# Kernel optimization log

Hardware: AMD Instinct MI355X
Metric: run time of the kernel (lower is better)

## Reference

```python
import jax, jax.numpy as jnp
import numpy as np

B, GNN_DIM, TR_DIM, F = 16384, 512, 768, 1024


def setup_inputs() -> dict:
    key = jax.random.key(0)
    ks = jax.random.split(key, 16)
    s = 0.02
    return {
        "gnn_features": jax.random.normal(ks[0], (B, GNN_DIM), jnp.float32),
        "transformer_features": jax.random.normal(ks[1], (B, TR_DIM), jnp.float32),
        # gnn_projector / transformer_projector (torch Linear: y = x @ W.T + b)
        "Wg": jax.random.normal(ks[2], (F, GNN_DIM), jnp.float32) * s,
        "bg": jnp.zeros((F,), jnp.float32),
        "Wt": jax.random.normal(ks[3], (F, TR_DIM), jnp.float32) * s,
        "bt": jnp.zeros((F,), jnp.float32),
        # MultiheadAttention value-projection slice of in_proj_weight and out_proj.
        # With seq_len==1 the softmax over a single key is identically 1, so the
        # attention output is exactly out_proj(v_proj(key)); Q/K projections do
        # not affect the output (their gradients are exactly zero).
        "Wv": jax.random.normal(ks[4], (F, F), jnp.float32) * s,
        "bv": jnp.zeros((F,), jnp.float32),
        "Wo": jax.random.normal(ks[5], (F, F), jnp.float32) * s,
        "bo": jnp.zeros((F,), jnp.float32),
        # fusion_layers: Linear(2F -> F), GELU, Dropout(eval: identity), Linear(F -> F)
        "W1": jax.random.normal(ks[6], (F, 2 * F), jnp.float32) * s,
        "b1": jnp.zeros((F,), jnp.float32),
        "W2": jax.random.normal(ks[7], (F, F), jnp.float32) * s,
        "b2": jnp.zeros((F,), jnp.float32),
    }


def reference(gnn_features, transformer_features, Wg, bg, Wt, bt, Wv, bv, Wo, bo, W1, b1, W2, b2):
    # projections to fusion space  [B, F]
    gnn_proj = gnn_features @ Wg.T + bg
    tr_proj = transformer_features @ Wt.T + bt
    # degenerate single-token cross-attention: softmax over 1 key == 1, so
    # attn(q, k, v=k) = out_proj(v_proj(k)) regardless of the query.
    gnn_attended = (tr_proj @ Wv.T + bv) @ Wo.T + bo   # attention(gnn_seq, tr_seq, tr_seq)
    tr_attended = (gnn_proj @ Wv.T + bv) @ Wo.T + bo   # attention(tr_seq, gnn_seq, gnn_seq)
    combined = jnp.concatenate([gnn_attended, tr_attended], axis=-1)  # [B, 2F]
    h = jax.nn.gelu(combined @ W1.T + b1, approximate=False)          # exact GELU (torch default)
    fused = h @ W2.T + b2
    return fused + gnn_proj + tr_proj
```

## Files before the change

kernel.cpp:

```cpp
#include <hip/hip_runtime.h>
#include <cmath>

#define GAS __attribute__((address_space(1)))
#define LAS __attribute__((address_space(3)))

typedef __bf16 bf16x8 __attribute__((ext_vector_type(8)));
typedef float f32x4 __attribute__((ext_vector_type(4)));

__device__ __forceinline__ void gload16(const void* g, void* l) {
    __builtin_amdgcn_global_load_lds((const GAS void*)g, (LAS void*)l, 16, 0, 0);
}

__global__ void k_prep_convert(const float* __restrict__ gnn, const float* __restrict__ tr,
                               const float* __restrict__ Wo, const float* __restrict__ W1,
                               const float* __restrict__ W2, const float* __restrict__ Wg,
                               const float* __restrict__ Wt,
                               __bf16* __restrict__ X, __bf16* __restrict__ Wo_b,
                               __bf16* __restrict__ W1ab, __bf16* __restrict__ Wp) {
    int b = blockIdx.x;
    const float* src; __bf16* dst; int sld, dld, base, c8;
    if (b < 4096)       { src = gnn;       sld = 512;  dst = X + 1024;        dld = 2304; base = 0;     c8 = 64; }
    else if (b < 10240) { src = tr;        sld = 768;  dst = X + 1536;        dld = 2304; base = 4096;  c8 = 96; }
    else if (b < 10752) { src = Wo;        sld = 1024; dst = Wo_b;            dld = 1024; base = 10240; c8 = 128; }
    else if (b < 11264) { src = W1;        sld = 2048; dst = W1ab;            dld = 1024; base = 10752; c8 = 128; }
    else if (b < 11776) { src = W1 + 1024; sld = 2048; dst = W1ab + 1024*1024; dld = 1024; base = 11264; c8 = 128; }
    else if (b < 12288) { src = W2;        sld = 1024; dst = Wp;              dld = 2304; base = 11776; c8 = 128; }
    else if (b < 12544) { src = Wg;        sld = 512;  dst = Wp + 1024;       dld = 2304; base = 12288; c8 = 64; }
    else                { src = Wt;        sld = 768;  dst = Wp + 1536;       dld = 2304; base = 12544; c8 = 96; }
    int idx = (b - base) * 256 + threadIdx.x;
    int r = idx / c8;
    int c = (idx - r * c8) << 3;
    const float4* s = reinterpret_cast<const float4*>(src + (long)r * sld + c);
    float4 x0 = s[0], x1 = s[1];
    bf16x8 v;
    v[0] = (__bf16)x0.x; v[1] = (__bf16)x0.y; v[2] = (__bf16)x0.z; v[3] = (__bf16)x0.w;
    v[4] = (__bf16)x1.x; v[5] = (__bf16)x1.y; v[6] = (__bf16)x1.z; v[7] = (__bf16)x1.w;
    *reinterpret_cast<bf16x8*>(dst + (long)r * dld + c) = v;
}

__global__ void k_prep_transpose(const float* __restrict__ Wv, const float* __restrict__ Wg,
                                 const float* __restrict__ Wt,
                                 __bf16* __restrict__ WvT, __bf16* __restrict__ WgT,
                                 __bf16* __restrict__ WtT) {
    __shared__ float t[32][33];
    int b = blockIdx.x;
    const float* src; __bf16* dst; int R, C, tile;
    if (b < 1024)      { src = Wv; dst = WvT; R = 1024; C = 1024; tile = b; }
    else if (b < 1536) { src = Wg; dst = WgT; R = 1024; C = 512;  tile = b - 1024; }
    else               { src = Wt; dst = WtT; R = 1024; C = 768;  tile = b - 1536; }
    int tx_n = C >> 5;
    int c0 = (tile % tx_n) << 5, r0 = (tile / tx_n) << 5;
    int tx = threadIdx.x, ty = threadIdx.y;
    #pragma unroll
    for (int i = 0; i < 32; i += 8)
        t[ty + i][tx] = src[(long)(r0 + ty + i) * C + c0 + tx];
    __syncthreads();
    #pragma unroll
    for (int i = 0; i < 32; i += 8)
        dst[(long)(c0 + ty + i) * R + r0 + tx] = (__bf16)t[tx][ty + i];
}

__global__ void k_bias_att(const float* __restrict__ Wo, const float* __restrict__ bv,
                           const float* __restrict__ bo, float* __restrict__ b_att) {
    int i = blockIdx.x;
    float s = 0.f;
    for (int k = threadIdx.x; k < 1024; k += 256) s += Wo[i * 1024 + k] * bv[k];
    __shared__ float red[256];
    red[threadIdx.x] = s;
    __syncthreads();
    for (int off = 128; off > 0; off >>= 1) {
        if (threadIdx.x < off) red[threadIdx.x] += red[threadIdx.x + off];
        __syncthreads();
    }
    if (threadIdx.x == 0) b_att[i] = red[0] + bo[i];
}

__global__ void k_bias_z2(const float* __restrict__ W1, const float* __restrict__ b_att,
                          const float* __restrict__ b1,
                          const __bf16* __restrict__ P, const __bf16* __restrict__ Q,
                          const float* __restrict__ bt, const float* __restrict__ bg,
                          const float* __restrict__ b2,
                          float* __restrict__ bz2, float* __restrict__ b_out) {
    int i = blockIdx.x;
    float s = 0.f;
    for (int k = threadIdx.x; k < 1024; k += 256) {
        s += (W1[(long)i * 2048 + k] + W1[(long)i * 2048 + 1024 + k]) * b_att[k];
        s += (float)P[i * 1024 + k] * bt[k];
        s += (float)Q[i * 1024 + k] * bg[k];
    }
    __shared__ float red[256];
    red[threadIdx.x] = s;
    __syncthreads();
    for (int off = 128; off > 0; off >>= 1) {
        if (threadIdx.x < off) red[threadIdx.x] += red[threadIdx.x + off];
        __syncthreads();
    }
    if (threadIdx.x == 0) {
        bz2[i] = red[0] + b1[i];
        b_out[i] = b2[i] + bg[i] + bt[i];
    }
}

template <int BM, int BN>
__global__ __launch_bounds__(256, 2) void k_gemm_nt(
    const __bf16* __restrict__ A, int lda,
    const __bf16* __restrict__ B, int ldb,
    __bf16* __restrict__ C, int ldc,
    int K, int n_tiles) {
    constexpr int BK = 32;
    constexpr int MR = BM / 32, NR = BN / 32;
    __shared__ alignas(16) __bf16 As[2][BM][BK];
    __shared__ alignas(16) __bf16 Bs[2][BN][BK];

    const int tid = threadIdx.x;
    const int lane = tid & 63;
    const int wave = tid >> 6;
    int bid = blockIdx.x;
    const int nwg = gridDim.x;
    if ((nwg & 7) == 0) bid = (bid & 7) * (nwg >> 3) + (bid >> 3);
    const int bn = bid % n_tiles;
    const int bm = bid / n_tiles;
    const int m0 = bm * BM, n0 = bn * BN;

    const int rp_l = tid >> 2;
    const int sp = tid & 3;

    const int wr = (wave >> 1) * (BM / 2);
    const int wc = (wave & 1) * (BN / 2);
    const int fr = lane & 15;
    const int fb = (lane >> 4) << 4;

    f32x4 acc[MR][NR] = {};
    const int nk = K / BK;

    auto stage = [&](int buf, int kt) {
        char* abase = (char*)&As[buf][0][0];
        char* bbase = (char*)&Bs[buf][0][0];
        #pragma unroll
        for (int it = 0; it < BM / 64; ++it) {
            int rp = it * 64 + rp_l;
            int rl = (rp & ~1) | ((rp ^ (rp >> 2)) & 1);
            int sl = sp ^ (rl & 3);
            gload16(A + (long)(m0 + rl) * lda + kt * BK + sl * 8,
                    abase + it * 4096 + tid * 16);
        }
        #pragma unroll
        for (int it = 0; it < BN / 64; ++it) {
            int rp = it * 64 + rp_l;
            int rl = (rp & ~1) | ((rp ^ (rp >> 2)) & 1);
            int sl = sp ^ (rl & 3);
            gload16(B + (long)(n0 + rl) * ldb + kt * BK + sl * 8,
                    bbase + it * 4096 + tid * 16);
        }
    };

    stage(0, 0);
    for (int kt = 0; kt < nk; ++kt) {
        const int buf = kt & 1;
        __syncthreads();
        if (kt + 1 < nk) stage(buf ^ 1, kt + 1);
        const char* abase = (const char*)&As[buf][0][0];
        const char* bbase = (const char*)&Bs[buf][0][0];
        bf16x8 af[MR], bfr[NR];
        #pragma unroll
        for (int m = 0; m < MR; ++m) {
            int r = wr + m * 16 + fr;
            af[m] = *(const bf16x8*)(abase + (((r << 6) + fb) ^ ((r & 7) << 4)));
        }
        #pragma unroll
        for (int n = 0; n < NR; ++n) {
            int r = wc + n * 16 + fr;
            bfr[n] = *(const bf16x8*)(bbase + (((r << 6) + fb) ^ ((r & 7) << 4)));
        }
        #pragma unroll
        for (int m = 0; m < MR; ++m)
            #pragma unroll
            for (int n = 0; n < NR; ++n)
                acc[m][n] = __builtin_amdgcn_mfma_f32_16x16x32_bf16(af[m], bfr[n], acc[m][n], 0, 0, 0);
    }

    const int r0 = (lane >> 4) << 2;
    #pragma unroll
    for (int n = 0; n < NR; ++n) {
        const int gc = n0 + wc + n * 16 + fr;
        #pragma unroll
        for (int m = 0; m < MR; ++m) {
            const long rbase = (long)(m0 + wr + m * 16 + r0);
            #pragma unroll
            for (int r = 0; r < 4; ++r)
                C[(rbase + r) * ldc + gc] = (__bf16)acc[m][n][r];
        }
    }
}

template <int MODE>
__device__ __forceinline__ void gemm8_body(
    const __bf16* __restrict__ A, int lda,
    const __bf16* __restrict__ B, int ldb,
    void* __restrict__ Cv, int ldc,
    const float* __restrict__ bias,
    int K, int n_tiles) {
    __shared__ char lds[131072];

    const int tid = threadIdx.x;
    const int lane = tid & 63;
    const int wave = tid >> 6;
    const int wm = wave >> 2;
    const int wn = wave & 3;

    int bid = blockIdx.x;
    const int nwg = gridDim.x;
    if ((nwg & 7) == 0) bid = (bid & 7) * (nwg >> 3) + (bid >> 3);
    const int bn = bid % n_tiles;
    const int bm = bid / n_tiles;
    const int m0 = bm * 256, n0 = bn * 256;

    const int rowA = ((tid >> 7) << 4) + (tid & 15);
    const int colA = (((tid >> 6) & 1) << 5) + (((tid >> 4) & 3) << 3);
    const int rowB = ((tid >> 6) << 4) + (tid & 15);
    const int colB = (((tid >> 4) & 3) << 3);
    const __bf16* Ag = A + (long)(m0 + rowA) * lda + colA;
    const __bf16* Bg = B + (long)(n0 + rowB) * ldb + colB;
    const int tid16 = tid * 16;
    const int l16 = lane * 16;
    const int fr = lane & 15;

    const int bnh = wn >> 1;
    const int bno = (wn & 1) * 4096;

    f32x4 acc[8][4] = {};
    bf16x8 af[4];
    bf16x8 bfr[2][4];

    const int nk = K >> 6;
    const int NI = nk >> 1;

#define STAGE_A(PAR, KT, MH, QH) \
    gload16(Ag + (long)(KT) * 64 + (long)((MH) * 128 + (QH) * 64) * lda, \
            lds + (PAR) * 32768 + (MH) * 16384 + (QH) * 8192 + tid16)
#define STAGE_B(PAR, KT, NH, KK) \
    gload16(Bg + (long)(KT) * 64 + (KK) * 32 + (long)((NH) * 128) * ldb, \
            lds + 65536 + (PAR) * 32768 + (NH) * 16384 + (KK) * 8192 + tid16)
#define VMC8 asm volatile("s_waitcnt vmcnt(8)" ::: "memory")
#define VMC6 asm volatile("s_waitcnt vmcnt(6)" ::: "memory")
#define VMC0 asm volatile("s_waitcnt vmcnt(0)" ::: "memory")
#define BAR  __builtin_amdgcn_s_barrier()
#define RD_A4(PAR, QH, KK) { \
        const char* a_ = lds + (PAR) * 32768 + wm * 16384 + (QH) * 8192 + (KK) * 1024; \
        _Pragma("unroll") \
        for (int m_ = 0; m_ < 4; ++m_) \
            af[m_] = *(const bf16x8*)(a_ + m_ * 2048 + l16); }
#define RD_B4(KK, PAR) { \
        const char* b_ = lds + 65536 + (PAR) * 32768 + bnh * 16384 + (KK) * 8192 + bno; \
        _Pragma("unroll") \
        for (int n_ = 0; n_ < 4; ++n_) \
            bfr[KK][n_] = *(const bf16x8*)(b_ + n_ * 1024 + l16); }
#define MFMA16(QH, KK) { \
        __builtin_amdgcn_s_setprio(1); \
        _Pragma("unroll") \
        for (int m_ = 0; m_ < 4; ++m_) { \
            _Pragma("unroll") \
            for (int n_ = 0; n_ < 4; ++n_) \
                acc[(QH) * 4 + m_][n_] = __builtin_amdgcn_mfma_f32_16x16x32_bf16( \
                    af[m_], bfr[KK][n_], acc[(QH) * 4 + m_][n_], 0, 0, 0); } \
        __builtin_amdgcn_s_setprio(0); }

    STAGE_A(0, 0, 0, 0); STAGE_A(0, 0, 1, 0);
    STAGE_B(0, 0, 0, 0); STAGE_B(0, 0, 1, 0);
    STAGE_A(0, 0, 0, 1); STAGE_A(0, 0, 1, 1);
    STAGE_B(0, 0, 0, 1); STAGE_B(0, 0, 1, 1);
    STAGE_A(1, 1, 0, 0); STAGE_A(1, 1, 1, 0);
    STAGE_B(1, 1, 0, 0); STAGE_B(1, 1, 1, 0);

    for (int I = 0; I < NI; ++I) {
        const int t = 2 * I;
        const bool nl = (I + 1 < NI);
        VMC8;
        STAGE_A(1, t + 1, 0, 1); STAGE_A(1, t + 1, 1, 1);
        BAR; RD_B4(0, 0); RD_A4(0, 0, 0); MFMA16(0, 0); BAR;
        VMC6;
        STAGE_B(1, t + 1, 0, 1); STAGE_B(1, t + 1, 1, 1);
        BAR; RD_B4(1, 0); RD_A4(0, 0, 1); MFMA16(0, 1); BAR;
        if (nl) { STAGE_A(0, t + 2, 0, 0); STAGE_A(0, t + 2, 1, 0); } else { VMC0; }
        BAR; RD_A4(0, 1, 0); MFMA16(1, 0); BAR;
        if (nl) { STAGE_B(0, t + 2, 0, 0); STAGE_B(0, t + 2, 1, 0); }
        BAR; RD_A4(0, 1, 1); MFMA16(1, 1); BAR;
        VMC8;
        if (nl) { STAGE_A(0, t + 2, 0, 1); STAGE_A(0, t + 2, 1, 1); }
        BAR; RD_B4(0, 1); RD_A4(1, 0, 0); MFMA16(0, 0); BAR;
        VMC6;
        if (nl) { STAGE_B(0, t + 2, 0, 1); STAGE_B(0, t + 2, 1, 1); }
        BAR; RD_B4(1, 1); RD_A4(1, 0, 1); MFMA16(0, 1); BAR;
        if (nl) { STAGE_A(1, t + 3, 0, 0); STAGE_A(1, t + 3, 1, 0); }
        BAR; RD_A4(1, 1, 0); MFMA16(1, 0); BAR;
        if (nl) { STAGE_B(1, t + 3, 0, 0); STAGE_B(1, t + 3, 1, 0); }
        BAR; RD_A4(1, 1, 1); MFMA16(1, 1); BAR;
    }
#undef MFMA16
#undef RD_B4
#undef RD_A4
#undef BAR
#undef VMC0
#undef VMC6
#undef VMC8
#undef STAGE_B
#undef STAGE_A

    char* scr = lds + wave * 16384;
    float bval[4];
    #pragma unroll
    for (int n_ = 0; n_ < 4; ++n_)
        bval[n_] = bias ? bias[n0 + wn * 64 + n_ * 16 + fr] : 0.0f;
    const int r0q = (lane >> 4) << 2;

    #pragma unroll
    for (int mq = 0; mq < 8; ++mq) {
        #pragma unroll
        for (int n_ = 0; n_ < 4; ++n_) {
            #pragma unroll
            for (int r = 0; r < 4; ++r) {
                float v = acc[mq][n_][r] + bval[n_];
                if (MODE == 1) {
                    float u = v * (0.7978845608f + 0.0356774081f * v * v);
                    float e = __expf(-2.0f * fabsf(u));
                    float th = (1.0f - e) / (1.0f + e);
                    th = copysignf(th, u);
                    v = 0.5f * v * (1.0f + th);
                }
                *(float*)(scr + (r0q + r) * 272 + (n_ * 16 + fr) * 4) = v;
            }
        }
        __builtin_amdgcn_s_waitcnt(0);
        if (MODE == 2) {
            #pragma unroll
            for (int rep = 0; rep < 4; ++rep) {
                int row = rep * 4 + (lane >> 4);
                f32x4 val = *(const f32x4*)(scr + row * 272 + (lane & 15) * 16);
                long grow = (long)(m0 + wm * 128 + mq * 16 + row);
                *(f32x4*)&((float*)Cv)[grow * ldc + n0 + wn * 64 + (lane & 15) * 4] = val;
            }
        } else {
            #pragma unroll
            for (int rep = 0; rep < 2; ++rep) {
                int row = rep * 8 + (lane >> 3);
                f32x4 v0 = *(const f32x4*)(scr + row * 272 + (lane & 7) * 32);
                f32x4 v1 = *(const f32x4*)(scr + row * 272 + (lane & 7) * 32 + 16);
                bf16x8 o;
                o[0] = (__bf16)v0[0]; o[1] = (__bf16)v0[1]; o[2] = (__bf16)v0[2]; o[3] = (__bf16)v0[3];
                o[4] = (__bf16)v1[0]; o[5] = (__bf16)v1[1]; o[6] = (__bf16)v1[2]; o[7] = (__bf16)v1[3];
                long grow = (long)(m0 + wm * 128 + mq * 16 + row);
                *(bf16x8*)&((__bf16*)Cv)[grow * ldc + n0 + wn * 64 + (lane & 7) * 8] = o;
            }
        }
        __builtin_amdgcn_s_waitcnt(0);
    }
}

__global__ __launch_bounds__(512, 2) void k_gemm8_gelu(
    const __bf16* __restrict__ A, int lda, const __bf16* __restrict__ B, int ldb,
    void* __restrict__ Cv, int ldc, const float* __restrict__ bias, int K, int n_tiles) {
    gemm8_body<1>(A, lda, B, ldb, Cv, ldc, bias, K, n_tiles);
}
__global__ __launch_bounds__(512, 2) void k_gemm8_out(
    const __bf16* __restrict__ A, int lda, const __bf16* __restrict__ B, int ldb,
    void* __restrict__ Cv, int ldc, const float* __restrict__ bias, int K, int n_tiles) {
    gemm8_body<2>(A, lda, B, ldb, Cv, ldc, bias, K, n_tiles);
}

extern "C" void kernel_launch(void* const* d_in, const int* in_sizes, int n_in,
                              void* d_out, int out_size, void* d_ws, size_t ws_size,
                              hipStream_t stream) {
    constexpr int Bsz = 16384, F = 1024, GD = 512, TD = 768;
    constexpr int XLD = F + GD + TD;

    const float* gnn = (const float*)d_in[0];
    const float* tr  = (const float*)d_in[1];
    const float* Wg  = (const float*)d_in[2];
    const float* bg  = (const float*)d_in[3];
    const float* Wt  = (const float*)d_in[4];
    const float* bt  = (const float*)d_in[5];
    const float* Wv  = (const float*)d_in[6];
    const float* bv  = (const float*)d_in[7];
    const float* Wo  = (const float*)d_in[8];
    const float* bo  = (const float*)d_in[9];
    const float* W1  = (const float*)d_in[10];
    const float* b1  = (const float*)d_in[11];
    const float* W2  = (const float*)d_in[12];
    const float* b2  = (const float*)d_in[13];
    float* out = (float*)d_out;

    char* w = (char*)d_ws;
    auto alloc = [&](size_t bytes) {
        char* p = w;
        w += (bytes + 255) & ~(size_t)255;
        return p;
    };
    __bf16* X    = (__bf16*)alloc((size_t)Bsz * XLD * 2);
    __bf16* M1   = (__bf16*)alloc((size_t)F * (GD + TD) * 2);
    __bf16* Wp   = (__bf16*)alloc((size_t)F * XLD * 2);
    __bf16* WvT  = (__bf16*)alloc((size_t)F * F * 2);
    __bf16* WgT  = (__bf16*)alloc((size_t)GD * F * 2);
    __bf16* WtT  = (__bf16*)alloc((size_t)TD * F * 2);
    __bf16* Wo_b = (__bf16*)alloc((size_t)F * F * 2);
    __bf16* W1ab = (__bf16*)alloc((size_t)2 * F * F * 2);
    __bf16* AT   = (__bf16*)alloc((size_t)F * F * 2);
    __bf16* PQ   = (__bf16*)alloc((size_t)2 * F * F * 2);
    float* b_att = (float*)alloc(F * 4);
    float* bz2   = (float*)alloc(F * 4);
    float* b_out = (float*)alloc(F * 4);
    if ((size_t)(w - (char*)d_ws) > ws_size) return;

    dim3 b256(256);
    __bf16* P = PQ;
    __bf16* Q = PQ + (size_t)F * F;

    k_prep_convert<<<dim3(12928), b256, 0, stream>>>(gnn, tr, Wo, W1, W2, Wg, Wt,
                                                     X, Wo_b, W1ab, Wp);
    k_prep_transpose<<<dim3(2304), dim3(32, 8), 0, stream>>>(Wv, Wg, Wt, WvT, WgT, WtT);
    k_bias_att<<<dim3(F), b256, 0, stream>>>(Wo, bv, bo, b_att);

    k_gemm_nt<64, 64><<<dim3((F / 64) * (F / 64)), b256, 0, stream>>>(
        WvT, F, Wo_b, F, AT, F, F, F / 64);
    k_gemm_nt<64, 64><<<dim3((2 * F / 64) * (F / 64)), b256, 0, stream>>>(
        W1ab, F, AT, F, PQ, F, F, F / 64);
    k_gemm_nt<64, 64><<<dim3((F / 64) * (GD / 64)), b256, 0, stream>>>(
        Q, F, WgT, F, M1, GD + TD, F, GD / 64);
    k_gemm_nt<64, 64><<<dim3((F / 64) * (TD / 64)), b256, 0, stream>>>(
        P, F, WtT, F, M1 + GD, GD + TD, F, TD / 64);

    k_bias_z2<<<dim3(F), b256, 0, stream>>>(W1, b_att, b1, P, Q, bt, bg, b2, bz2, b_out);

    k_gemm8_gelu<<<dim3((Bsz / 256) * (F / 256)), dim3(512), 0, stream>>>(
        X + F, XLD, M1, GD + TD, X, XLD, bz2, GD + TD, F / 256);

    k_gemm8_out<<<dim3((Bsz / 256) * (F / 256)), dim3(512), 0, stream>>>(
        X, XLD, Wp, XLD, out, F, b_out, XLD, F / 256);
}
```

Baseline: 225.9 us.

## Issue LDS fragment reads before barrier and retune vmcnt waits in GEMM loop

Reorders the pipelined GEMM main loop so each phase's LDS fragment reads are issued before the workgroup barrier, pinned with a sched_barrier, and the MFMAs then run between barriers. It also replaces the vmcnt(8)/vmcnt(6) wait pattern with vmcnt(4)/vmcnt(6) at new points and adds a prologue wait plus barrier. The aim is to hide LDS read latency and bring the global-to-LDS wait accounting in line with the new order. The risk is a race if the reads now run ahead of the barrier that guarantees the staged data has landed, and the tighter waits may stall more often.

```diff
diff --git a/kernel.cpp b/kernel.cpp
--- a/kernel.cpp
+++ b/kernel.cpp
@@ -241,10 +241,11 @@
 #define STAGE_B(PAR, KT, NH, KK) \
     gload16(Bg + (long)(KT) * 64 + (KK) * 32 + (long)((NH) * 128) * ldb, \
             lds + 65536 + (PAR) * 32768 + (NH) * 16384 + (KK) * 8192 + tid16)
-#define VMC8 asm volatile("s_waitcnt vmcnt(8)" ::: "memory")
 #define VMC6 asm volatile("s_waitcnt vmcnt(6)" ::: "memory")
+#define VMC4 asm volatile("s_waitcnt vmcnt(4)" ::: "memory")
 #define VMC0 asm volatile("s_waitcnt vmcnt(0)" ::: "memory")
 #define BAR  __builtin_amdgcn_s_barrier()
+#define PIN  __builtin_amdgcn_sched_barrier(0)
 #define RD_A4(PAR, QH, KK) { \
         const char* a_ = lds + (PAR) * 32768 + wm * 16384 + (QH) * 8192 + (KK) * 1024; \
         _Pragma("unroll") \
@@ -271,38 +272,48 @@
     STAGE_B(0, 0, 0, 1); STAGE_B(0, 0, 1, 1);
     STAGE_A(1, 1, 0, 0); STAGE_A(1, 1, 1, 0);
     STAGE_B(1, 1, 0, 0); STAGE_B(1, 1, 1, 0);
+    VMC4;
+    BAR;
 
     for (int I = 0; I < NI; ++I) {
         const int t = 2 * I;
         const bool nl = (I + 1 < NI);
-        VMC8;
+        VMC4;
         STAGE_A(1, t + 1, 0, 1); STAGE_A(1, t + 1, 1, 1);
-        BAR; RD_B4(0, 0); RD_A4(0, 0, 0); MFMA16(0, 0); BAR;
-        VMC6;
+        RD_B4(0, 0); RD_A4(0, 0, 0); PIN;
+        BAR; MFMA16(0, 0); BAR;
         STAGE_B(1, t + 1, 0, 1); STAGE_B(1, t + 1, 1, 1);
-        BAR; RD_B4(1, 0); RD_A4(0, 0, 1); MFMA16(0, 1); BAR;
-        if (nl) { STAGE_A(0, t + 2, 0, 0); STAGE_A(0, t + 2, 1, 0); } else { VMC0; }
-        BAR; RD_A4(0, 1, 0); MFMA16(1, 0); BAR;
-        if (nl) { STAGE_B(0, t + 2, 0, 0); STAGE_B(0, t + 2, 1, 0); }
-        BAR; RD_A4(0, 1, 1); MFMA16(1, 1); BAR;
-        VMC8;
+        RD_B4(1, 0); RD_A4(0, 0, 1); PIN;
+        BAR; MFMA16(0, 1); BAR;
+        if (nl) { STAGE_A(0, t + 2, 0, 0); STAGE_A(0, t + 2, 1, 0); }
+        RD_A4(0, 1, 0); PIN;
+        BAR; MFMA16(1, 0); BAR;
+        if (nl) { VMC6; STAGE_B(0, t + 2, 0, 0); STAGE_B(0, t + 2, 1, 0); } else { VMC0; }
+        RD_A4(0, 1, 1); PIN;
+        BAR; MFMA16(1, 1); BAR;
+        VMC4;
         if (nl) { STAGE_A(0, t + 2, 0, 1); STAGE_A(0, t + 2, 1, 1); }
-        BAR; RD_B4(0, 1); RD_A4(1, 0, 0); MFMA16(0, 0); BAR;
-        VMC6;
+        RD_B4(0, 1); RD_A4(1, 0, 0); PIN;
+        BAR; MFMA16(0, 0); BAR;
         if (nl) { STAGE_B(0, t + 2, 0, 1); STAGE_B(0, t + 2, 1, 1); }
-        BAR; RD_B4(1, 1); RD_A4(1, 0, 1); MFMA16(0, 1); BAR;
+        RD_B4(1, 1); RD_A4(1, 0, 1); PIN;
+        BAR; MFMA16(0, 1); BAR;
         if (nl) { STAGE_A(1, t + 3, 0, 0); STAGE_A(1, t + 3, 1, 0); }
-        BAR; RD_A4(1, 1, 0); MFMA16(1, 0); BAR;
+        RD_A4(1, 1, 0); PIN;
+        BAR; MFMA16(1, 0); BAR;
+        VMC4;
         if (nl) { STAGE_B(1, t + 3, 0, 0); STAGE_B(1, t + 3, 1, 0); }
-        BAR; RD_A4(1, 1, 1); MFMA16(1, 1); BAR;
+        RD_A4(1, 1, 1); PIN;
+        BAR; MFMA16(1, 1); BAR;
     }
 #undef MFMA16
 #undef RD_B4
 #undef RD_A4
+#undef PIN
 #undef BAR
 #undef VMC0
+#undef VMC4
 #undef VMC6
-#undef VMC8
 #undef STAGE_B
 #undef STAGE_A
 
```

Result: no change. 229.0 us (+1.4%).

## Switch big GEMMs to 32x32x16 MFMA and reassociate weight-folding chain into two fused launches

Applied to the files above, without the earlier changes.

The two large batch GEMMs now use 32x32x16 bf16 MFMA tiles instead of 16x16x32. This cuts the number of LDS fragment reads per MFMA and changes the epilogue row mapping to match. The weight-folding precompute is reassociated: W1 halves are multiplied by Wo^T first, then by Wv-projected Wg/Wt. This collapses four dependent small GEMM launches into two batched kernels, and the prep and bias kernels are merged. The risks are added register pressure from the larger accumulators and a different bf16 rounding order in the folded weights.

```diff
diff --git a/kernel.cpp b/kernel.cpp
--- a/kernel.cpp
+++ b/kernel.cpp
@@ -6,65 +6,73 @@
 
 typedef __bf16 bf16x8 __attribute__((ext_vector_type(8)));
 typedef float f32x4 __attribute__((ext_vector_type(4)));
+typedef float f32x16 __attribute__((ext_vector_type(16)));
 
 __device__ __forceinline__ void gload16(const void* g, void* l) {
     __builtin_amdgcn_global_load_lds((const GAS void*)g, (LAS void*)l, 16, 0, 0);
 }
 
-__global__ void k_prep_convert(const float* __restrict__ gnn, const float* __restrict__ tr,
-                               const float* __restrict__ Wo, const float* __restrict__ W1,
-                               const float* __restrict__ W2, const float* __restrict__ Wg,
-                               const float* __restrict__ Wt,
-                               __bf16* __restrict__ X, __bf16* __restrict__ Wo_b,
-                               __bf16* __restrict__ W1ab, __bf16* __restrict__ Wp) {
-    int b = blockIdx.x;
-    const float* src; __bf16* dst; int sld, dld, base, c8;
-    if (b < 4096)       { src = gnn;       sld = 512;  dst = X + 1024;        dld = 2304; base = 0;     c8 = 64; }
-    else if (b < 10240) { src = tr;        sld = 768;  dst = X + 1536;        dld = 2304; base = 4096;  c8 = 96; }
-    else if (b < 10752) { src = Wo;        sld = 1024; dst = Wo_b;            dld = 1024; base = 10240; c8 = 128; }
-    else if (b < 11264) { src = W1;        sld = 2048; dst = W1ab;            dld = 1024; base = 10752; c8 = 128; }
-    else if (b < 11776) { src = W1 + 1024; sld = 2048; dst = W1ab + 1024*1024; dld = 1024; base = 11264; c8 = 128; }
-    else if (b < 12288) { src = W2;        sld = 1024; dst = Wp;              dld = 2304; base = 11776; c8 = 128; }
-    else if (b < 12544) { src = Wg;        sld = 512;  dst = Wp + 1024;       dld = 2304; base = 12288; c8 = 64; }
-    else                { src = Wt;        sld = 768;  dst = Wp + 1536;       dld = 2304; base = 12544; c8 = 96; }
-    int idx = (b - base) * 256 + threadIdx.x;
-    int r = idx / c8;
-    int c = (idx - r * c8) << 3;
-    const float4* s = reinterpret_cast<const float4*>(src + (long)r * sld + c);
-    float4 x0 = s[0], x1 = s[1];
-    bf16x8 v;
-    v[0] = (__bf16)x0.x; v[1] = (__bf16)x0.y; v[2] = (__bf16)x0.z; v[3] = (__bf16)x0.w;
-    v[4] = (__bf16)x1.x; v[5] = (__bf16)x1.y; v[6] = (__bf16)x1.z; v[7] = (__bf16)x1.w;
-    *reinterpret_cast<bf16x8*>(dst + (long)r * dld + c) = v;
-}
-
-__global__ void k_prep_transpose(const float* __restrict__ Wv, const float* __restrict__ Wg,
-                                 const float* __restrict__ Wt,
-                                 __bf16* __restrict__ WvT, __bf16* __restrict__ WgT,
-                                 __bf16* __restrict__ WtT) {
+__global__ void k_prep(const float* __restrict__ gnn, const float* __restrict__ tr,
+                       const float* __restrict__ Wo, const float* __restrict__ W1,
+                       const float* __restrict__ W2, const float* __restrict__ Wg,
+                       const float* __restrict__ Wt, const float* __restrict__ Wv,
+                       __bf16* __restrict__ X, __bf16* __restrict__ W1ab,
+                       __bf16* __restrict__ Wp, __bf16* __restrict__ Wv_b,
+                       __bf16* __restrict__ WoT, __bf16* __restrict__ WgT,
+                       __bf16* __restrict__ WtT) {
     __shared__ float t[32][33];
     int b = blockIdx.x;
-    const float* src; __bf16* dst; int R, C, tile;
-    if (b < 1024)      { src = Wv; dst = WvT; R = 1024; C = 1024; tile = b; }
-    else if (b < 1536) { src = Wg; dst = WgT; R = 1024; C = 512;  tile = b - 1024; }
-    else               { src = Wt; dst = WtT; R = 1024; C = 768;  tile = b - 1536; }
-    int tx_n = C >> 5;
-    int c0 = (tile % tx_n) << 5, r0 = (tile / tx_n) << 5;
-    int tx = threadIdx.x, ty = threadIdx.y;
-    #pragma unroll
-    for (int i = 0; i < 32; i += 8)
-        t[ty + i][tx] = src[(long)(r0 + ty + i) * C + c0 + tx];
-    __syncthreads();
-    #pragma unroll
-    for (int i = 0; i < 32; i += 8)
-        dst[(long)(c0 + ty + i) * R + r0 + tx] = (__bf16)t[tx][ty + i];
-}
-
-__global__ void k_bias_att(const float* __restrict__ Wo, const float* __restrict__ bv,
-                           const float* __restrict__ bo, float* __restrict__ b_att) {
-    int i = blockIdx.x;
+    int tid = threadIdx.x;
+    if (b < 12928) {
+        const float* src; __bf16* dst; int sld, dld, base, c8;
+        if (b < 4096)       { src=gnn;     sld=512;  dst=X+1024;         dld=2304; base=0;     c8=64; }
+        else if (b < 10240) { src=tr;      sld=768;  dst=X+1536;         dld=2304; base=4096;  c8=96; }
+        else if (b < 10752) { src=W1;      sld=2048; dst=W1ab;           dld=1024; base=10240; c8=128; }
+        else if (b < 11264) { src=W1+1024; sld=2048; dst=W1ab+1024*1024; dld=1024; base=10752; c8=128; }
+        else if (b < 11776) { src=W2;      sld=1024; dst=Wp;             dld=2304; base=11264; c8=128; }
+        else if (b < 12032) { src=Wg;      sld=512;  dst=Wp+1024;        dld=2304; base=11776; c8=64; }
+        else if (b < 12416) { src=Wt;      sld=768;  dst=Wp+1536;        dld=2304; base=12032; c8=96; }
+        else                { src=Wv;      sld=1024; dst=Wv_b;           dld=1024; base=12416; c8=128; }
+        int idx = (b - base) * 256 + tid;
+        int r = idx / c8;
+        int c = (idx - r * c8) << 3;
+        const float4* s = reinterpret_cast<const float4*>(src + (long)r * sld + c);
+        float4 x0 = s[0], x1 = s[1];
+        bf16x8 v;
+        v[0]=(__bf16)x0.x; v[1]=(__bf16)x0.y; v[2]=(__bf16)x0.z; v[3]=(__bf16)x0.w;
+        v[4]=(__bf16)x1.x; v[5]=(__bf16)x1.y; v[6]=(__bf16)x1.z; v[7]=(__bf16)x1.w;
+        *reinterpret_cast<bf16x8*>(dst + (long)r * dld + c) = v;
+    } else {
+        int bb = b - 12928;
+        const float* src; __bf16* dst; int R, C, tile;
+        if (bb < 1024)      { src=Wo; dst=WoT; R=1024; C=1024; tile=bb; }
+        else if (bb < 1536) { src=Wg; dst=WgT; R=1024; C=512;  tile=bb-1024; }
+        else                { src=Wt; dst=WtT; R=1024; C=768;  tile=bb-1536; }
+        int tx_n = C >> 5;
+        int c0 = (tile % tx_n) << 5, r0 = (tile / tx_n) << 5;
+        int tx = tid & 31, ty = tid >> 5;
+        #pragma unroll
+        for (int i = 0; i < 32; i += 8)
+            t[ty + i][tx] = src[(long)(r0 + ty + i) * C + c0 + tx];
+        __syncthreads();
+        #pragma unroll
+        for (int i = 0; i < 32; i += 8)
+            dst[(long)(c0 + ty + i) * R + r0 + tx] = (__bf16)t[tx][ty + i];
+    }
+}
+
+__global__ void k_bias1(const float* __restrict__ Wo, const float* __restrict__ bv,
+                        const float* __restrict__ bo, const float* __restrict__ Wv,
+                        const float* __restrict__ bt, const float* __restrict__ bg,
+                        float* __restrict__ b_att, float* __restrict__ vb_t,
+                        float* __restrict__ vb_g) {
+    int b = blockIdx.x;
+    const float* mat; const float* vec; float* dst; int i; bool addbo = false;
+    if (b < 1024)      { mat = Wo; vec = bv; dst = b_att; i = b;        addbo = true; }
+    else if (b < 2048) { mat = Wv; vec = bt; dst = vb_t;  i = b - 1024; }
+    else               { mat = Wv; vec = bg; dst = vb_g;  i = b - 2048; }
     float s = 0.f;
-    for (int k = threadIdx.x; k < 1024; k += 256) s += Wo[i * 1024 + k] * bv[k];
+    for (int k = threadIdx.x; k < 1024; k += 256) s += mat[(long)i * 1024 + k] * vec[k];
     __shared__ float red[256];
     red[threadIdx.x] = s;
     __syncthreads();
@@ -72,12 +80,12 @@
         if (threadIdx.x < off) red[threadIdx.x] += red[threadIdx.x + off];
         __syncthreads();
     }
-    if (threadIdx.x == 0) b_att[i] = red[0] + bo[i];
+    if (threadIdx.x == 0) dst[i] = red[0] + (addbo ? bo[i] : 0.f);
 }
 
 __global__ void k_bias_z2(const float* __restrict__ W1, const float* __restrict__ b_att,
-                          const float* __restrict__ b1,
-                          const __bf16* __restrict__ P, const __bf16* __restrict__ Q,
+                          const float* __restrict__ b1, const __bf16* __restrict__ U12,
+                          const float* __restrict__ vb_t, const float* __restrict__ vb_g,
                           const float* __restrict__ bt, const float* __restrict__ bg,
                           const float* __restrict__ b2,
                           float* __restrict__ bz2, float* __restrict__ b_out) {
@@ -85,8 +93,8 @@
     float s = 0.f;
     for (int k = threadIdx.x; k < 1024; k += 256) {
         s += (W1[(long)i * 2048 + k] + W1[(long)i * 2048 + 1024 + k]) * b_att[k];
-        s += (float)P[i * 1024 + k] * bt[k];
-        s += (float)Q[i * 1024 + k] * bg[k];
+        s += (float)U12[(long)i * 1024 + k] * vb_t[k];
+        s += (float)U12[(long)(i + 1024) * 1024 + k] * vb_g[k];
     }
     __shared__ float red[256];
     red[threadIdx.x] = s;
@@ -101,32 +109,27 @@
     }
 }
 
-template <int BM, int BN>
-__global__ __launch_bounds__(256, 2) void k_gemm_nt(
+__device__ __forceinline__ void gemm64_body(
     const __bf16* __restrict__ A, int lda,
     const __bf16* __restrict__ B, int ldb,
     __bf16* __restrict__ C, int ldc,
-    int K, int n_tiles) {
-    constexpr int BK = 32;
-    constexpr int MR = BM / 32, NR = BN / 32;
+    int K, int n_tiles, int bid) {
+    constexpr int BM = 64, BN = 64, BK = 32;
+    constexpr int MR = 2, NR = 2;
     __shared__ alignas(16) __bf16 As[2][BM][BK];
     __shared__ alignas(16) __bf16 Bs[2][BN][BK];
 
     const int tid = threadIdx.x;
     const int lane = tid & 63;
     const int wave = tid >> 6;
-    int bid = blockIdx.x;
-    const int nwg = gridDim.x;
-    if ((nwg & 7) == 0) bid = (bid & 7) * (nwg >> 3) + (bid >> 3);
     const int bn = bid % n_tiles;
     const int bm = bid / n_tiles;
     const int m0 = bm * BM, n0 = bn * BN;
 
     const int rp_l = tid >> 2;
     const int sp = tid & 3;
-
-    const int wr = (wave >> 1) * (BM / 2);
-    const int wc = (wave & 1) * (BN / 2);
+    const int wr = (wave >> 1) * 32;
+    const int wc = (wave & 1) * 32;
     const int fr = lane & 15;
     const int fb = (lane >> 4) << 4;
 
@@ -134,24 +137,10 @@
     const int nk = K / BK;
 
     auto stage = [&](int buf, int kt) {
-        char* abase = (char*)&As[buf][0][0];
-        char* bbase = (char*)&Bs[buf][0][0];
-        #pragma unroll
-        for (int it = 0; it < BM / 64; ++it) {
-            int rp = it * 64 + rp_l;
-            int rl = (rp & ~1) | ((rp ^ (rp >> 2)) & 1);
-            int sl = sp ^ (rl & 3);
-            gload16(A + (long)(m0 + rl) * lda + kt * BK + sl * 8,
-                    abase + it * 4096 + tid * 16);
-        }
-        #pragma unroll
-        for (int it = 0; it < BN / 64; ++it) {
-            int rp = it * 64 + rp_l;
-            int rl = (rp & ~1) | ((rp ^ (rp >> 2)) & 1);
-            int sl = sp ^ (rl & 3);
-            gload16(B + (long)(n0 + rl) * ldb + kt * BK + sl * 8,
-                    bbase + it * 4096 + tid * 16);
-        }
+        int rl = (rp_l & ~1) | ((rp_l ^ (rp_l >> 2)) & 1);
+        int sl = sp ^ (rl & 3);
+        gload16(A + (long)(m0 + rl) * lda + kt * BK + sl * 8, (char*)&As[buf][0][0] + tid * 16);
+        gload16(B + (long)(n0 + rl) * ldb + kt * BK + sl * 8, (char*)&Bs[buf][0][0] + tid * 16);
     };
 
     stage(0, 0);
@@ -193,6 +182,25 @@
     }
 }
 
+__global__ __launch_bounds__(256, 2) void k_gemmL1(
+    const __bf16* __restrict__ W1ab, const __bf16* __restrict__ WoT,
+    const __bf16* __restrict__ WtT, const __bf16* __restrict__ WgT,
+    const __bf16* __restrict__ Wv_b, __bf16* __restrict__ U12,
+    __bf16* __restrict__ VtT, __bf16* __restrict__ VgT) {
+    int b = blockIdx.x;
+    if (b < 512)      gemm64_body(W1ab, 1024, WoT, 1024, U12, 1024, 1024, 16, b);
+    else if (b < 704) gemm64_body(WtT, 1024, Wv_b, 1024, VtT, 1024, 1024, 16, b - 512);
+    else              gemm64_body(WgT, 1024, Wv_b, 1024, VgT, 1024, 1024, 16, b - 704);
+}
+
+__global__ __launch_bounds__(256, 2) void k_gemmL2(
+    const __bf16* __restrict__ U12, const __bf16* __restrict__ VtT,
+    const __bf16* __restrict__ VgT, __bf16* __restrict__ M1) {
+    int b = blockIdx.x;
+    if (b < 192) gemm64_body(U12, 1024, VtT, 1024, M1 + 512, 1280, 1024, 12, b);
+    else         gemm64_body(U12 + 1024 * 1024, 1024, VgT, 1024, M1, 1280, 1024, 8, b - 192);
+}
+
 template <int MODE>
 __device__ __forceinline__ void gemm8_body(
     const __bf16* __restrict__ A, int lda,
@@ -222,15 +230,15 @@
     const __bf16* Ag = A + (long)(m0 + rowA) * lda + colA;
     const __bf16* Bg = B + (long)(n0 + rowB) * ldb + colB;
     const int tid16 = tid * 16;
-    const int l16 = lane * 16;
-    const int fr = lane & 15;
-
+
+    const int laneA = ((lane >> 4) & 1) * 2048 + (lane >> 5) * 256 + (lane & 15) * 16;
+    const int laneB = ((lane >> 4) & 1) * 1024 + (lane >> 5) * 256 + (lane & 15) * 16;
     const int bnh = wn >> 1;
     const int bno = (wn & 1) * 4096;
 
-    f32x4 acc[8][4] = {};
-    bf16x8 af[4];
-    bf16x8 bfr[2][4];
+    f32x16 acc[4][2] = {};
+    bf16x8 af[2][2];
+    bf16x8 bfr[2][2][2];
 
     const int nk = K >> 6;
     const int NI = nk >> 1;
@@ -245,24 +253,30 @@
 #define VMC6 asm volatile("s_waitcnt vmcnt(6)" ::: "memory")
 #define VMC0 asm volatile("s_waitcnt vmcnt(0)" ::: "memory")
 #define BAR  __builtin_amdgcn_s_barrier()
-#define RD_A4(PAR, QH, KK) { \
+#define RD_A32(PAR, QH, KK) { \
         const char* a_ = lds + (PAR) * 32768 + wm * 16384 + (QH) * 8192 + (KK) * 1024; \
         _Pragma("unroll") \
-        for (int m_ = 0; m_ < 4; ++m_) \
-            af[m_] = *(const bf16x8*)(a_ + m_ * 2048 + l16); }
-#define RD_B4(KK, PAR) { \
+        for (int fm_ = 0; fm_ < 2; ++fm_) { \
+            _Pragma("unroll") \
+            for (int h_ = 0; h_ < 2; ++h_) \
+                af[fm_][h_] = *(const bf16x8*)(a_ + fm_ * 4096 + h_ * 512 + laneA); } }
+#define RD_B32(KK, PAR) { \
         const char* b_ = lds + 65536 + (PAR) * 32768 + bnh * 16384 + (KK) * 8192 + bno; \
         _Pragma("unroll") \
-        for (int n_ = 0; n_ < 4; ++n_) \
-            bfr[KK][n_] = *(const bf16x8*)(b_ + n_ * 1024 + l16); }
-#define MFMA16(QH, KK) { \
+        for (int fn_ = 0; fn_ < 2; ++fn_) { \
+            _Pragma("unroll") \
+            for (int h_ = 0; h_ < 2; ++h_) \
+                bfr[KK][h_][fn_] = *(const bf16x8*)(b_ + fn_ * 2048 + h_ * 512 + laneB); } }
+#define MFMA8(QH, KK) { \
         __builtin_amdgcn_s_setprio(1); \
         _Pragma("unroll") \
-        for (int m_ = 0; m_ < 4; ++m_) { \
+        for (int h_ = 0; h_ < 2; ++h_) { \
             _Pragma("unroll") \
-            for (int n_ = 0; n_ < 4; ++n_) \
-                acc[(QH) * 4 + m_][n_] = __builtin_amdgcn_mfma_f32_16x16x32_bf16( \
-                    af[m_], bfr[KK][n_], acc[(QH) * 4 + m_][n_], 0, 0, 0); } \
+            for (int fm_ = 0; fm_ < 2; ++fm_) { \
+                _Pragma("unroll") \
+                for (int fn_ = 0; fn_ < 2; ++fn_) \
+                    acc[(QH) * 2 + fm_][fn_] = __builtin_amdgcn_mfma_f32_32x32x16_bf16( \
+                        af[fm_][h_], bfr[KK][h_][fn_], acc[(QH) * 2 + fm_][fn_], 0, 0, 0); } } \
         __builtin_amdgcn_s_setprio(0); }
 
     STAGE_A(0, 0, 0, 0); STAGE_A(0, 0, 1, 0);
@@ -277,28 +291,28 @@
         const bool nl = (I + 1 < NI);
         VMC8;
         STAGE_A(1, t + 1, 0, 1); STAGE_A(1, t + 1, 1, 1);
-        BAR; RD_B4(0, 0); RD_A4(0, 0, 0); MFMA16(0, 0); BAR;
+        BAR; RD_B32(0, 0); RD_A32(0, 0, 0); MFMA8(0, 0); BAR;
         VMC6;
         STAGE_B(1, t + 1, 0, 1); STAGE_B(1, t + 1, 1, 1);
-        BAR; RD_B4(1, 0); RD_A4(0, 0, 1); MFMA16(0, 1); BAR;
+        BAR; RD_B32(1, 0); RD_A32(0, 0, 1); MFMA8(0, 1); BAR;
         if (nl) { STAGE_A(0, t + 2, 0, 0); STAGE_A(0, t + 2, 1, 0); } else { VMC0; }
-        BAR; RD_A4(0, 1, 0); MFMA16(1, 0); BAR;
+        BAR; RD_A32(0, 1, 0); MFMA8(1, 0); BAR;
         if (nl) { STAGE_B(0, t + 2, 0, 0); STAGE_B(0, t + 2, 1, 0); }
-        BAR; RD_A4(0, 1, 1); MFMA16(1, 1); BAR;
+        BAR; RD_A32(0, 1, 1); MFMA8(1, 1); BAR;
         VMC8;
         if (nl) { STAGE_A(0, t + 2, 0, 1); STAGE_A(0, t + 2, 1, 1); }
-        BAR; RD_B4(0, 1); RD_A4(1, 0, 0); MFMA16(0, 0); BAR;
+        BAR; RD_B32(0, 1); RD_A32(1, 0, 0); MFMA8(0, 0); BAR;
         VMC6;
         if (nl) { STAGE_B(0, t + 2, 0, 1); STAGE_B(0, t + 2, 1, 1); }
-        BAR; RD_B4(1, 1); RD_A4(1, 0, 1); MFMA16(0, 1); BAR;
+        BAR; RD_B32(1, 1); RD_A32(1, 0, 1); MFMA8(0, 1); BAR;
         if (nl) { STAGE_A(1, t + 3, 0, 0); STAGE_A(1, t + 3, 1, 0); }
-        BAR; RD_A4(1, 1, 0); MFMA16(1, 0); BAR;
+        BAR; RD_A32(1, 1, 0); MFMA8(1, 0); BAR;
         if (nl) { STAGE_B(1, t + 3, 0, 0); STAGE_B(1, t + 3, 1, 0); }
-        BAR; RD_A4(1, 1, 1); MFMA16(1, 1); BAR;
-    }
-#undef MFMA16
-#undef RD_B4
-#undef RD_A4
+        BAR; RD_A32(1, 1, 1); MFMA8(1, 1); BAR;
+    }
+#undef MFMA8
+#undef RD_B32
+#undef RD_A32
 #undef BAR
 #undef VMC0
 #undef VMC6
@@ -307,19 +321,19 @@
 #undef STAGE_A
 
     char* scr = lds + wave * 16384;
-    float bval[4];
+    const int col32 = lane & 31;
+    const int rb5 = (lane >> 5) << 2;
+    float bval[2];
+    bval[0] = bias ? bias[n0 + wn * 64 + col32] : 0.0f;
+    bval[1] = bias ? bias[n0 + wn * 64 + 32 + col32] : 0.0f;
+
     #pragma unroll
-    for (int n_ = 0; n_ < 4; ++n_)
-        bval[n_] = bias ? bias[n0 + wn * 64 + n_ * 16 + fr] : 0.0f;
-    const int r0q = (lane >> 4) << 2;
-
-    #pragma unroll
-    for (int mq = 0; mq < 8; ++mq) {
-        #pragma unroll
-        for (int n_ = 0; n_ < 4; ++n_) {
+    for (int FM = 0; FM < 4; ++FM) {
+        #pragma unroll
+        for (int fn_ = 0; fn_ < 2; ++fn_) {
             #pragma unroll
-            for (int r = 0; r < 4; ++r) {
-                float v = acc[mq][n_][r] + bval[n_];
+            for (int rg = 0; rg < 16; ++rg) {
+                float v = acc[FM][fn_][rg] + bval[fn_];
                 if (MODE == 1) {
                     float u = v * (0.7978845608f + 0.0356774081f * v * v);
                     float e = __expf(-2.0f * fabsf(u));
@@ -327,41 +341,42 @@
                     th = copysignf(th, u);
                     v = 0.5f * v * (1.0f + th);
                 }
-                *(float*)(scr + (r0q + r) * 272 + (n_ * 16 + fr) * 4) = v;
+                int srow = (rg & 3) + ((rg >> 2) << 3) + rb5;
+                *(float*)(scr + srow * 272 + (fn_ * 32 + col32) * 4) = v;
             }
         }
-        __builtin_amdgcn_s_waitcnt(0);
+        asm volatile("s_waitcnt lgkmcnt(0)" ::: "memory");
         if (MODE == 2) {
             #pragma unroll
-            for (int rep = 0; rep < 4; ++rep) {
+            for (int rep = 0; rep < 8; ++rep) {
                 int row = rep * 4 + (lane >> 4);
                 f32x4 val = *(const f32x4*)(scr + row * 272 + (lane & 15) * 16);
-                long grow = (long)(m0 + wm * 128 + mq * 16 + row);
+                long grow = (long)(m0 + wm * 128 + FM * 32 + row);
                 *(f32x4*)&((float*)Cv)[grow * ldc + n0 + wn * 64 + (lane & 15) * 4] = val;
             }
         } else {
             #pragma unroll
-            for (int rep = 0; rep < 2; ++rep) {
+            for (int rep = 0; rep < 4; ++rep) {
                 int row = rep * 8 + (lane >> 3);
                 f32x4 v0 = *(const f32x4*)(scr + row * 272 + (lane & 7) * 32);
                 f32x4 v1 = *(const f32x4*)(scr + row * 272 + (lane & 7) * 32 + 16);
                 bf16x8 o;
                 o[0] = (__bf16)v0[0]; o[1] = (__bf16)v0[1]; o[2] = (__bf16)v0[2]; o[3] = (__bf16)v0[3];
                 o[4] = (__bf16)v1[0]; o[5] = (__bf16)v1[1]; o[6] = (__bf16)v1[2]; o[7] = (__bf16)v1[3];
-                long grow = (long)(m0 + wm * 128 + mq * 16 + row);
+                long grow = (long)(m0 + wm * 128 + FM * 32 + row);
                 *(bf16x8*)&((__bf16*)Cv)[grow * ldc + n0 + wn * 64 + (lane & 7) * 8] = o;
             }
         }
-        __builtin_amdgcn_s_waitcnt(0);
-    }
-}
-
-__global__ __launch_bounds__(512, 2) void k_gemm8_gelu(
+        asm volatile("s_waitcnt lgkmcnt(0)" ::: "memory");
+    }
+}
+
+__global__ __launch_bounds__(512, 2) void k_g256_gelu(
     const __bf16* __restrict__ A, int lda, const __bf16* __restrict__ B, int ldb,
     void* __restrict__ Cv, int ldc, const float* __restrict__ bias, int K, int n_tiles) {
     gemm8_body<1>(A, lda, B, ldb, Cv, ldc, bias, K, n_tiles);
 }
-__global__ __launch_bounds__(512, 2) void k_gemm8_out(
+__global__ __launch_bounds__(512, 2) void k_g256_out(
     const __bf16* __restrict__ A, int lda, const __bf16* __restrict__ B, int ldb,
     void* __restrict__ Cv, int ldc, const float* __restrict__ bias, int K, int n_tiles) {
     gemm8_body<2>(A, lda, B, ldb, Cv, ldc, bias, K, n_tiles);
@@ -398,41 +413,37 @@
     __bf16* X    = (__bf16*)alloc((size_t)Bsz * XLD * 2);
     __bf16* M1   = (__bf16*)alloc((size_t)F * (GD + TD) * 2);
     __bf16* Wp   = (__bf16*)alloc((size_t)F * XLD * 2);
-    __bf16* WvT  = (__bf16*)alloc((size_t)F * F * 2);
+    __bf16* W1ab = (__bf16*)alloc((size_t)2 * F * F * 2);
+    __bf16* Wv_b = (__bf16*)alloc((size_t)F * F * 2);
+    __bf16* WoT  = (__bf16*)alloc((size_t)F * F * 2);
     __bf16* WgT  = (__bf16*)alloc((size_t)GD * F * 2);
     __bf16* WtT  = (__bf16*)alloc((size_t)TD * F * 2);
-    __bf16* Wo_b = (__bf16*)alloc((size_t)F * F * 2);
-    __bf16* W1ab = (__bf16*)alloc((size_t)2 * F * F * 2);
-    __bf16* AT   = (__bf16*)alloc((size_t)F * F * 2);
-    __bf16* PQ   = (__bf16*)alloc((size_t)2 * F * F * 2);
+    __bf16* U12  = (__bf16*)alloc((size_t)2 * F * F * 2);
+    __bf16* VtT  = (__bf16*)alloc((size_t)TD * F * 2);
+    __bf16* VgT  = (__bf16*)alloc((size_t)GD * F * 2);
     float* b_att = (float*)alloc(F * 4);
+    float* vb_t  = (float*)alloc(F * 4);
+    float* vb_g  = (float*)alloc(F * 4);
     float* bz2   = (float*)alloc(F * 4);
     float* b_out = (float*)alloc(F * 4);
     if ((size_t)(w - (char*)d_ws) > ws_size) return;
 
     dim3 b256(256);
-    __bf16* P = PQ;
-    __bf16* Q = PQ + (size_t)F * F;
-
-    k_prep_convert<<<dim3(12928), b256, 0, stream>>>(gnn, tr, Wo, W1, W2, Wg, Wt,
-                                                     X, Wo_b, W1ab, Wp);
-    k_prep_transpose<<<dim3(2304), dim3(32, 8), 0, stream>>>(Wv, Wg, Wt, WvT, WgT, WtT);
-    k_bias_att<<<dim3(F), b256, 0, stream>>>(Wo, bv, bo, b_att);
-
-    k_gemm_nt<64, 64><<<dim3((F / 64) * (F / 64)), b256, 0, stream>>>(
-        WvT, F, Wo_b, F, AT, F, F, F / 64);
-    k_gemm_nt<64, 64><<<dim3((2 * F / 64) * (F / 64)), b256, 0, stream>>>(
-        W1ab, F, AT, F, PQ, F, F, F / 64);
-    k_gemm_nt<64, 64><<<dim3((F / 64) * (GD / 64)), b256, 0, stream>>>(
-        Q, F, WgT, F, M1, GD + TD, F, GD / 64);
-    k_gemm_nt<64, 64><<<dim3((F / 64) * (TD / 64)), b256, 0, stream>>>(
-        P, F, WtT, F, M1 + GD, GD + TD, F, TD / 64);
-
-    k_bias_z2<<<dim3(F), b256, 0, stream>>>(W1, b_att, b1, P, Q, bt, bg, b2, bz2, b_out);
-
-    k_gemm8_gelu<<<dim3((Bsz / 256) * (F / 256)), dim3(512), 0, stream>>>(
+
+    k_prep<<<dim3(15232), b256, 0, stream>>>(gnn, tr, Wo, W1, W2, Wg, Wt, Wv,
+                                             X, W1ab, Wp, Wv_b, WoT, WgT, WtT);
+    k_bias1<<<dim3(3072), b256, 0, stream>>>(Wo, bv, bo, Wv, bt, bg, b_att, vb_t, vb_g);
+
+    k_gemmL1<<<dim3(832), b256, 0, stream>>>(W1ab, WoT, WtT, WgT, Wv_b, U12, VtT, VgT);
+
+    k_bias_z2<<<dim3(F), b256, 0, stream>>>(W1, b_att, b1, U12, vb_t, vb_g, bt, bg, b2,
+                                            bz2, b_out);
+
+    k_gemmL2<<<dim3(320), b256, 0, stream>>>(U12, VtT, VgT, M1);
+
+    k_g256_gelu<<<dim3((Bsz / 256) * (F / 256)), dim3(512), 0, stream>>>(
         X + F, XLD, M1, GD + TD, X, XLD, bz2, GD + TD, F / 256);
 
-    k_gemm8_out<<<dim3((Bsz / 256) * (F / 256)), dim3(512), 0, stream>>>(
+    k_g256_out<<<dim3((Bsz / 256) * (F / 256)), dim3(512), 0, stream>>>(
         X, XLD, Wp, XLD, out, F, b_out, XLD, F / 256);
 }
```

Measured after the change: 217.2 us. 1.04x faster.
